# Performance work log

Measured on AMD Instinct MI355X. Metric: run time of the kernel, lower is better.

## Reference

```python
import jax, jax.numpy as jnp
import numpy as np
import math

N_CLASSES = 1000
CODE_LENGTH = 1024
IN_FEATURES = 4096
BATCH = 512
MAX_PROB = 0.95
POWER = 1.0


def _hadamard(n):
    # Sylvester construction; n must be a power of 2.
    H = np.array([[1.0]], dtype=np.float64)
    while H.shape[0] < n:
        H = np.block([[H, H], [H, -H]])
    return H


def setup_inputs() -> dict:
    key = jax.random.key(0)
    k1, k2, k3 = jax.random.split(key, 3)
    x = jax.random.normal(k1, (BATCH, IN_FEATURES), dtype=jnp.float32)
    out_feat = CODE_LENGTH - 1  # single head: code_length//1 - 1
    # nn.Linear default init: U(-1/sqrt(fan_in), 1/sqrt(fan_in))
    bound = 1.0 / math.sqrt(IN_FEATURES)
    W = jax.random.uniform(k2, (out_feat, IN_FEATURES), dtype=jnp.float32, minval=-bound, maxval=bound)
    b = jax.random.uniform(k3, (out_feat,), dtype=jnp.float32, minval=-bound, maxval=bound)
    labels = jnp.asarray(_hadamard(CODE_LENGTH)[:N_CLASSES, 1:], dtype=jnp.float32)  # (C, L-1)
    eps = jnp.float32(CODE_LENGTH * math.pow((1.0 - MAX_PROB) / (MAX_PROB * (N_CLASSES - 1)), 1.0 / POWER))
    power = jnp.float32(POWER)
    return {"x": x, "W": W, "b": b, "labels": labels, "eps": eps, "power": power}


def reference(x, W, b, labels, eps, power):
    # Linear head: (B, in) @ (in, L-1) + b
    h = jnp.tanh(x @ W.T + b)                               # (B, L-1)
    # L1 distance to each Hadamard code row: (B, 1, L-1) vs (C, L-1)
    d = jnp.sum(jnp.abs(h[:, None, :] - labels), axis=-1)   # (B, C)
    d = jnp.maximum(d, eps)
    inv = 1.0 / jnp.power(d, power)                          # (B, C)
    return inv / jnp.sum(inv, axis=-1, keepdims=True)
```

## Files before the change

### kernel.cpp

```cpp
#include <hip/hip_runtime.h>

#define BATCH 512
#define INFEAT 4096
#define LOUT 1023
#define NCLS 1000
#define NPAD 1024
#define SPLITK 8

typedef __bf16 bf16x8 __attribute__((ext_vector_type(8)));
typedef float f32x4 __attribute__((ext_vector_type(4)));

__device__ __forceinline__ unsigned short f2bf(float a) {
    unsigned u = __builtin_bit_cast(unsigned, a);
    return (unsigned short)((u + 0x7fffu + ((u >> 16) & 1u)) >> 16);
}
__device__ __forceinline__ float bf2f(unsigned short u) {
    return __builtin_bit_cast(float, ((unsigned)u) << 16);
}

__device__ __forceinline__ uint4 pack8(float4 a, float4 b) {
    union { __bf16 h[8]; uint4 u; } r;
    r.h[0] = (__bf16)a.x; r.h[1] = (__bf16)a.y;
    r.h[2] = (__bf16)a.z; r.h[3] = (__bf16)a.w;
    r.h[4] = (__bf16)b.x; r.h[5] = (__bf16)b.y;
    r.h[6] = (__bf16)b.z; r.h[7] = (__bf16)b.w;
    return r.u;
}

__global__ __launch_bounds__(256, 2) void k_gemm(
    const float* __restrict__ x, const float* __restrict__ W,
    unsigned short* __restrict__ partial) {
    __shared__ unsigned char lds[49152];
    const int bid = blockIdx.x;
    const int work = (bid & 7) * 64 + (bid >> 3);
    const int bn = work & 15, bm = (work >> 4) & 3, sp = work >> 6;
    const int tid = threadIdx.x;
    const int wave = tid >> 6, lane = tid & 63;
    const int lrow = lane & 15, lgrp = lane >> 4;
    const int wr = wave >> 1, wc = wave & 1;
    const int arow0 = bm * 128, brow0 = bn * 64, chunk0 = sp * 8;

    f32x4 acc[4][2] = {};
    float4 ar[4][2], br[2][2];

    auto LOADR = [&](int t) {
        const int c = chunk0 + t;
#pragma unroll
        for (int rr = 0; rr < 4; ++rr) {
            int g = rr * 256 + tid;
            int row = g >> 3, j = g & 7;
            const float4* p = (const float4*)(x + (size_t)(arow0 + row) * INFEAT
                                              + c * 64 + j * 8);
            ar[rr][0] = p[0]; ar[rr][1] = p[1];
        }
#pragma unroll
        for (int rr = 0; rr < 2; ++rr) {
            int g = rr * 256 + tid;
            int row = g >> 3, j = g & 7;
            int wrow = brow0 + row;
            if (wrow < LOUT) {
                const float4* p = (const float4*)(W + (size_t)wrow * INFEAT
                                                  + c * 64 + j * 8);
                br[rr][0] = p[0]; br[rr][1] = p[1];
            } else {
                br[rr][0] = make_float4(0.f, 0.f, 0.f, 0.f);
                br[rr][1] = make_float4(0.f, 0.f, 0.f, 0.f);
            }
        }
    };

    auto WRITE = [&](int bsel) {
        unsigned char* lA = lds + bsel * 24576;
        unsigned char* lB = lA + 16384;
#pragma unroll
        for (int rr = 0; rr < 4; ++rr) {
            int g = rr * 256 + tid;
            int row = g >> 3, j = g & 7;
            *(uint4*)(lA + row * 128 + ((j ^ (row & 7)) * 16)) =
                pack8(ar[rr][0], ar[rr][1]);
        }
#pragma unroll
        for (int rr = 0; rr < 2; ++rr) {
            int g = rr * 256 + tid;
            int row = g >> 3, j = g & 7;
            *(uint4*)(lB + row * 128 + ((j ^ (row & 7)) * 16)) =
                pack8(br[rr][0], br[rr][1]);
        }
    };

    auto COMPUTE = [&](int bsel) {
        const unsigned char* lA = lds + bsel * 24576;
        const unsigned char* lB = lA + 16384;
#pragma unroll
        for (int ks = 0; ks < 2; ++ks) {
            int swz = ((ks * 4 + lgrp) ^ (lrow & 7)) * 16;
            bf16x8 a[4], b[2];
#pragma unroll
            for (int m = 0; m < 4; ++m)
                a[m] = *(const bf16x8*)(lA + (wr * 64 + m * 16 + lrow) * 128 + swz);
#pragma unroll
            for (int n = 0; n < 2; ++n)
                b[n] = *(const bf16x8*)(lB + (wc * 32 + n * 16 + lrow) * 128 + swz);
#pragma unroll
            for (int m = 0; m < 4; ++m)
#pragma unroll
                for (int n = 0; n < 2; ++n)
                    acc[m][n] = __builtin_amdgcn_mfma_f32_16x16x32_bf16(
                        a[m], b[n], acc[m][n], 0, 0, 0);
        }
    };

    LOADR(0);
    WRITE(0);
    __syncthreads();
#pragma unroll 1
    for (int t = 0; t < 8; ++t) {
        if (t + 1 < 8) LOADR(t + 1);
        COMPUTE(t & 1);
        if (t + 1 < 8) WRITE((t + 1) & 1);
        __syncthreads();
    }

    unsigned short* P = partial + (size_t)sp * (BATCH * NPAD);
#pragma unroll
    for (int m = 0; m < 4; ++m)
#pragma unroll
        for (int n = 0; n < 2; ++n)
#pragma unroll
            for (int reg = 0; reg < 4; ++reg) {
                int r = arow0 + wr * 64 + m * 16 + lgrp * 4 + reg;
                int c = brow0 + wc * 32 + n * 16 + lrow;
                P[(size_t)r * NPAD + c] = f2bf(acc[m][n][reg]);
            }
}

__global__ __launch_bounds__(256) void k_fused(const unsigned short* __restrict__ partial,
                                               const float* __restrict__ bias,
                                               const float* __restrict__ epsp,
                                               const float* __restrict__ powp,
                                               float* __restrict__ out) {
    __shared__ float g[1024];
    __shared__ float wsum[4];
    const int r = blockIdx.x, t = threadIdx.x;
    const int n0 = t * 4;

    f32x4 v = {0.0f, 0.0f, 0.0f, 0.0f};
#pragma unroll
    for (int s = 0; s < SPLITK; ++s) {
        ushort4 p = *(const ushort4*)(partial + ((size_t)s * BATCH + r) * NPAD + n0);
        v[0] += bf2f(p.x); v[1] += bf2f(p.y); v[2] += bf2f(p.z); v[3] += bf2f(p.w);
    }
    float bb[4];
    if (t < 255) {
        float4 b4 = *(const float4*)(bias + n0);
        bb[0] = b4.x; bb[1] = b4.y; bb[2] = b4.z; bb[3] = b4.w;
    } else {
        bb[0] = bias[1020]; bb[1] = bias[1021]; bb[2] = bias[1022]; bb[3] = 0.0f;
    }
    if (t == 0) g[0] = 0.0f;
#pragma unroll
    for (int j = 0; j < 4; ++j) {
        int n = n0 + j;
        if (n < LOUT) g[n + 1] = tanhf(v[j] + bb[j]);
    }
    __syncthreads();

#pragma unroll 1
    for (int s = 0; s < 10; ++s) {
        int st = 1 << s;
#pragma unroll
        for (int pp = 0; pp < 2; ++pp) {
            int p = t + pp * 256;
            int idx = ((p >> s) << (s + 1)) | (p & (st - 1));
            float a = g[idx], c = g[idx + st];
            g[idx] = a + c;
            g[idx + st] = a - c;
        }
        __syncthreads();
    }

    const float eps = *epsp, pw = *powp;
    float iv[4];
    float ss = 0.0f;
#pragma unroll
    for (int j = 0; j < 4; ++j) {
        int c = n0 + j;
        float d = fmaxf(1023.0f - g[c], eps);
        float q = (pw == 1.0f) ? (1.0f / d) : powf(d, -pw);
        if (c >= NCLS) q = 0.0f;
        iv[j] = q;
        ss += q;
    }
#pragma unroll
    for (int m = 32; m; m >>= 1) ss += __shfl_xor(ss, m, 64);
    if ((t & 63) == 0) wsum[t >> 6] = ss;
    __syncthreads();
    float sc = 1.0f / (wsum[0] + wsum[1] + wsum[2] + wsum[3]);

    if (n0 < NCLS) {
        float4 o;
        o.x = iv[0] * sc; o.y = iv[1] * sc; o.z = iv[2] * sc; o.w = iv[3] * sc;
        *(float4*)(out + (size_t)r * NCLS + n0) = o;
    }
}

extern "C" void kernel_launch(void* const* d_in, const int* in_sizes, int n_in,
                              void* d_out, int out_size, void* d_ws, size_t ws_size,
                              hipStream_t stream) {
    const float* x = (const float*)d_in[0];
    const float* W = (const float*)d_in[1];
    const float* b = (const float*)d_in[2];
    const float* epsp = (const float*)d_in[4];
    const float* powp = (const float*)d_in[5];
    float* out = (float*)d_out;

    unsigned char* ws = (unsigned char*)d_ws;
    unsigned short* partial = (unsigned short*)ws;

    k_gemm<<<512, 256, 0, stream>>>(x, W, partial);
    k_fused<<<512, 256, 0, stream>>>(partial, b, epsp, powp, out);
}
```

Baseline: 26.83 us.

## Enlarge GEMM tile to 128x128 with 8 waves and three-stage register prefetch

The GEMM block grows to 512 threads covering a 128x128 output tile, which halves the grid to 256 blocks. The main loop becomes a fully unrolled schedule with two register staging sets, so global loads run two chunks ahead, fenced by explicit waitcnt, sched_barrier and s_barrier. MFMA sections are wrapped in raised s_setprio. The aim is more reuse of each A/B tile and better hiding of global load latency, at the cost of one block per CU and more registers per thread, with fewer blocks than the 256 CUs leave room to overlap.

```diff
diff --git a/kernel.cpp b/kernel.cpp
--- a/kernel.cpp
+++ b/kernel.cpp
@@ -17,7 +17,6 @@
 __device__ __forceinline__ float bf2f(unsigned short u) {
     return __builtin_bit_cast(float, ((unsigned)u) << 16);
 }
-
 __device__ __forceinline__ uint4 pack8(float4 a, float4 b) {
     union { __bf16 h[8]; uint4 u; } r;
     r.h[0] = (__bf16)a.x; r.h[1] = (__bf16)a.y;
@@ -27,70 +26,71 @@
     return r.u;
 }
 
-__global__ __launch_bounds__(256, 2) void k_gemm(
+__global__ __launch_bounds__(512, 1) void k_gemm(
     const float* __restrict__ x, const float* __restrict__ W,
     unsigned short* __restrict__ partial) {
-    __shared__ unsigned char lds[49152];
+    __shared__ unsigned char lds[65536];
     const int bid = blockIdx.x;
-    const int work = (bid & 7) * 64 + (bid >> 3);
-    const int bn = work & 15, bm = (work >> 4) & 3, sp = work >> 6;
+    const int work = (bid & 7) * 32 + (bid >> 3);
+    const int bn = work & 7, bm = (work >> 3) & 3, sp = work >> 5;
     const int tid = threadIdx.x;
     const int wave = tid >> 6, lane = tid & 63;
     const int lrow = lane & 15, lgrp = lane >> 4;
-    const int wr = wave >> 1, wc = wave & 1;
-    const int arow0 = bm * 128, brow0 = bn * 64, chunk0 = sp * 8;
+    const int wr = wave >> 2, wc = wave & 3;
+    const int arow0 = bm * 128, brow0 = bn * 128, chunk0 = sp * 8;
+
+    const int p0 = tid, p1 = 512 + tid;
+    const int row0 = p0 >> 3, jb0 = p0 & 7;
+    const int row1 = p1 >> 3, jb1 = p1 & 7;
 
     f32x4 acc[4][2] = {};
-    float4 ar[4][2], br[2][2];
-
-    auto LOADR = [&](int t) {
-        const int c = chunk0 + t;
-#pragma unroll
-        for (int rr = 0; rr < 4; ++rr) {
-            int g = rr * 256 + tid;
-            int row = g >> 3, j = g & 7;
-            const float4* p = (const float4*)(x + (size_t)(arow0 + row) * INFEAT
-                                              + c * 64 + j * 8);
-            ar[rr][0] = p[0]; ar[rr][1] = p[1];
-        }
-#pragma unroll
-        for (int rr = 0; rr < 2; ++rr) {
-            int g = rr * 256 + tid;
-            int row = g >> 3, j = g & 7;
-            int wrow = brow0 + row;
+    float4 sAa[4], sAb[4], sBa[4], sBb[4];
+
+    auto LOADR = [&](int t, float4 (&aa)[4], float4 (&bb)[4]) {
+        const size_t c0 = (size_t)(chunk0 + t) * 64;
+        {
+            const float4* q = (const float4*)(x + (size_t)(arow0 + row0) * INFEAT + c0 + jb0 * 8);
+            aa[0] = q[0]; aa[1] = q[1];
+        }
+        {
+            const float4* q = (const float4*)(x + (size_t)(arow0 + row1) * INFEAT + c0 + jb1 * 8);
+            aa[2] = q[0]; aa[3] = q[1];
+        }
+        {
+            int wrow = brow0 + row0;
             if (wrow < LOUT) {
-                const float4* p = (const float4*)(W + (size_t)wrow * INFEAT
-                                                  + c * 64 + j * 8);
-                br[rr][0] = p[0]; br[rr][1] = p[1];
+                const float4* q = (const float4*)(W + (size_t)wrow * INFEAT + c0 + jb0 * 8);
+                bb[0] = q[0]; bb[1] = q[1];
             } else {
-                br[rr][0] = make_float4(0.f, 0.f, 0.f, 0.f);
-                br[rr][1] = make_float4(0.f, 0.f, 0.f, 0.f);
+                bb[0] = make_float4(0.f, 0.f, 0.f, 0.f);
+                bb[1] = make_float4(0.f, 0.f, 0.f, 0.f);
             }
         }
+        {
+            int wrow = brow0 + row1;
+            if (wrow < LOUT) {
+                const float4* q = (const float4*)(W + (size_t)wrow * INFEAT + c0 + jb1 * 8);
+                bb[2] = q[0]; bb[3] = q[1];
+            } else {
+                bb[2] = make_float4(0.f, 0.f, 0.f, 0.f);
+                bb[3] = make_float4(0.f, 0.f, 0.f, 0.f);
+            }
+        }
     };
 
-    auto WRITE = [&](int bsel) {
-        unsigned char* lA = lds + bsel * 24576;
+    auto WRITE = [&](int bsel, float4 (&aa)[4], float4 (&bb)[4]) {
+        unsigned char* lA = lds + bsel * 32768;
         unsigned char* lB = lA + 16384;
-#pragma unroll
-        for (int rr = 0; rr < 4; ++rr) {
-            int g = rr * 256 + tid;
-            int row = g >> 3, j = g & 7;
-            *(uint4*)(lA + row * 128 + ((j ^ (row & 7)) * 16)) =
-                pack8(ar[rr][0], ar[rr][1]);
-        }
-#pragma unroll
-        for (int rr = 0; rr < 2; ++rr) {
-            int g = rr * 256 + tid;
-            int row = g >> 3, j = g & 7;
-            *(uint4*)(lB + row * 128 + ((j ^ (row & 7)) * 16)) =
-                pack8(br[rr][0], br[rr][1]);
-        }
+        *(uint4*)(lA + row0 * 128 + ((jb0 ^ (row0 & 7)) * 16)) = pack8(aa[0], aa[1]);
+        *(uint4*)(lA + row1 * 128 + ((jb1 ^ (row1 & 7)) * 16)) = pack8(aa[2], aa[3]);
+        *(uint4*)(lB + row0 * 128 + ((jb0 ^ (row0 & 7)) * 16)) = pack8(bb[0], bb[1]);
+        *(uint4*)(lB + row1 * 128 + ((jb1 ^ (row1 & 7)) * 16)) = pack8(bb[2], bb[3]);
     };
 
     auto COMPUTE = [&](int bsel) {
-        const unsigned char* lA = lds + bsel * 24576;
+        const unsigned char* lA = lds + bsel * 32768;
         const unsigned char* lB = lA + 16384;
+        __builtin_amdgcn_s_setprio(1);
 #pragma unroll
         for (int ks = 0; ks < 2; ++ks) {
             int swz = ((ks * 4 + lgrp) ^ (lrow & 7)) * 16;
@@ -108,18 +108,38 @@
                     acc[m][n] = __builtin_amdgcn_mfma_f32_16x16x32_bf16(
                         a[m], b[n], acc[m][n], 0, 0, 0);
         }
+        __builtin_amdgcn_s_setprio(0);
     };
 
-    LOADR(0);
-    WRITE(0);
-    __syncthreads();
-#pragma unroll 1
-    for (int t = 0; t < 8; ++t) {
-        if (t + 1 < 8) LOADR(t + 1);
-        COMPUTE(t & 1);
-        if (t + 1 < 8) WRITE((t + 1) & 1);
-        __syncthreads();
-    }
+    LOADR(0, sAa, sAb);
+    LOADR(1, sBa, sBb);
+    asm volatile("s_waitcnt vmcnt(8)" ::: "memory");
+    __builtin_amdgcn_sched_barrier(0);
+    WRITE(0, sAa, sAb);
+    LOADR(2, sAa, sAb);
+    asm volatile("s_waitcnt lgkmcnt(0)" ::: "memory");
+    __builtin_amdgcn_sched_barrier(0);
+    __builtin_amdgcn_s_barrier();
+
+#define STEP(T, SA, SB, VMC)                                          \
+    COMPUTE(T & 1);                                                   \
+    asm volatile("s_waitcnt vmcnt(" #VMC ")" ::: "memory");           \
+    __builtin_amdgcn_sched_barrier(0);                                \
+    WRITE((T + 1) & 1, SA, SB);                                       \
+    if ((T) <= 4) LOADR((T) + 3, SA, SB);                             \
+    asm volatile("s_waitcnt lgkmcnt(0)" ::: "memory");                \
+    __builtin_amdgcn_sched_barrier(0);                                \
+    __builtin_amdgcn_s_barrier();
+
+    STEP(0, sBa, sBb, 8)
+    STEP(1, sAa, sAb, 8)
+    STEP(2, sBa, sBb, 8)
+    STEP(3, sAa, sAb, 8)
+    STEP(4, sBa, sBb, 8)
+    STEP(5, sAa, sAb, 8)
+    STEP(6, sBa, sBb, 0)
+    COMPUTE(1);
+#undef STEP
 
     unsigned short* P = partial + (size_t)sp * (BATCH * NPAD);
 #pragma unroll
@@ -217,6 +237,6 @@
     unsigned char* ws = (unsigned char*)d_ws;
     unsigned short* partial = (unsigned short*)ws;
 
-    k_gemm<<<512, 256, 0, stream>>>(x, W, partial);
+    k_gemm<<<256, 512, 0, stream>>>(x, W, partial);
     k_fused<<<512, 256, 0, stream>>>(partial, b, epsp, powp, out);
 }
```

New measurement: 25.92 us. -3.4%, faster.

## Stage full W slice in LDS once and stream x fragments directly into registers

Applied to the files above, without the earlier changes.

The GEMM kernel now uses 256 blocks of 512 threads, each with a 128x128 output tile over a 512-wide K slice. The whole bf16 W slice (128 KB) is loaded into LDS up front with one barrier. The x operand is loaded straight from global memory into MFMA fragment registers, using a three-deep register prefetch ring. This removes the per-step LDS double-buffering and its barriers, at the cost of occupancy limited to one block per CU, a large LDS footprint, and uncoalesced per-lane x loads that each block re-reads from global memory.

```diff
diff --git a/kernel.cpp b/kernel.cpp
--- a/kernel.cpp
+++ b/kernel.cpp
@@ -6,6 +6,8 @@
 #define NCLS 1000
 #define NPAD 1024
 #define SPLITK 8
+#define KSLICE 512
+#define NCHUNK 16
 
 typedef __bf16 bf16x8 __attribute__((ext_vector_type(8)));
 typedef float f32x4 __attribute__((ext_vector_type(4)));
@@ -17,109 +19,88 @@
 __device__ __forceinline__ float bf2f(unsigned short u) {
     return __builtin_bit_cast(float, ((unsigned)u) << 16);
 }
-
-__device__ __forceinline__ uint4 pack8(float4 a, float4 b) {
-    union { __bf16 h[8]; uint4 u; } r;
+__device__ __forceinline__ bf16x8 pack8(float4 a, float4 b) {
+    union { __bf16 h[8]; bf16x8 v; } r;
     r.h[0] = (__bf16)a.x; r.h[1] = (__bf16)a.y;
     r.h[2] = (__bf16)a.z; r.h[3] = (__bf16)a.w;
     r.h[4] = (__bf16)b.x; r.h[5] = (__bf16)b.y;
     r.h[6] = (__bf16)b.z; r.h[7] = (__bf16)b.w;
-    return r.u;
-}
-
-__global__ __launch_bounds__(256, 2) void k_gemm(
+    return r.v;
+}
+
+__global__ __launch_bounds__(512, 1) void k_gemm(
     const float* __restrict__ x, const float* __restrict__ W,
     unsigned short* __restrict__ partial) {
-    __shared__ unsigned char lds[49152];
+    __shared__ unsigned char lB[128 * 1024];
     const int bid = blockIdx.x;
-    const int work = (bid & 7) * 64 + (bid >> 3);
-    const int bn = work & 15, bm = (work >> 4) & 3, sp = work >> 6;
+    const int work = (bid & 7) * 32 + (bid >> 3);
+    const int bn = work & 7, bm = (work >> 3) & 3, sp = work >> 5;
     const int tid = threadIdx.x;
     const int wave = tid >> 6, lane = tid & 63;
     const int lrow = lane & 15, lgrp = lane >> 4;
-    const int wr = wave >> 1, wc = wave & 1;
-    const int arow0 = bm * 128, brow0 = bn * 64, chunk0 = sp * 8;
+    const int wr = wave >> 2, wc = wave & 3;
+    const int arow0 = bm * 128, brow0 = bn * 128;
+    const size_t c0 = (size_t)sp * KSLICE;
+
+    {
+        const int r = tid >> 2, s = tid & 3;
+        const int wrow = brow0 + r;
+        const float* src = W + (size_t)wrow * INFEAT + c0 + s * 128;
+        unsigned char* dst = lB + r * 1024;
+#pragma unroll
+        for (int i = 0; i < 16; ++i) {
+            float4 v0, v1;
+            if (wrow < LOUT) {
+                v0 = *(const float4*)(src + i * 8);
+                v1 = *(const float4*)(src + i * 8 + 4);
+            } else {
+                v0 = make_float4(0.f, 0.f, 0.f, 0.f);
+                v1 = v0;
+            }
+            *(bf16x8*)(dst + (((s * 16 + i) ^ (r & 7)) * 16)) = pack8(v0, v1);
+        }
+    }
+    __syncthreads();
 
     f32x4 acc[4][2] = {};
-    float4 ar[4][2], br[2][2];
-
-    auto LOADR = [&](int t) {
-        const int c = chunk0 + t;
-#pragma unroll
-        for (int rr = 0; rr < 4; ++rr) {
-            int g = rr * 256 + tid;
-            int row = g >> 3, j = g & 7;
-            const float4* p = (const float4*)(x + (size_t)(arow0 + row) * INFEAT
-                                              + c * 64 + j * 8);
-            ar[rr][0] = p[0]; ar[rr][1] = p[1];
-        }
-#pragma unroll
-        for (int rr = 0; rr < 2; ++rr) {
-            int g = rr * 256 + tid;
-            int row = g >> 3, j = g & 7;
-            int wrow = brow0 + row;
-            if (wrow < LOUT) {
-                const float4* p = (const float4*)(W + (size_t)wrow * INFEAT
-                                                  + c * 64 + j * 8);
-                br[rr][0] = p[0]; br[rr][1] = p[1];
-            } else {
-                br[rr][0] = make_float4(0.f, 0.f, 0.f, 0.f);
-                br[rr][1] = make_float4(0.f, 0.f, 0.f, 0.f);
-            }
+    float4 A0[4][2], A1[4][2], A2[4][2];
+
+    auto LOADA = [&](int kk, float4 (&S)[4][2]) {
+#pragma unroll
+        for (int m = 0; m < 4; ++m) {
+            const float4* q = (const float4*)(x +
+                (size_t)(arow0 + wr * 64 + m * 16 + lrow) * INFEAT +
+                c0 + kk * 32 + lgrp * 8);
+            S[m][0] = q[0]; S[m][1] = q[1];
         }
     };
 
-    auto WRITE = [&](int bsel) {
-        unsigned char* lA = lds + bsel * 24576;
-        unsigned char* lB = lA + 16384;
-#pragma unroll
-        for (int rr = 0; rr < 4; ++rr) {
-            int g = rr * 256 + tid;
-            int row = g >> 3, j = g & 7;
-            *(uint4*)(lA + row * 128 + ((j ^ (row & 7)) * 16)) =
-                pack8(ar[rr][0], ar[rr][1]);
-        }
-#pragma unroll
-        for (int rr = 0; rr < 2; ++rr) {
-            int g = rr * 256 + tid;
-            int row = g >> 3, j = g & 7;
-            *(uint4*)(lB + row * 128 + ((j ^ (row & 7)) * 16)) =
-                pack8(br[rr][0], br[rr][1]);
-        }
-    };
-
-    auto COMPUTE = [&](int bsel) {
-        const unsigned char* lA = lds + bsel * 24576;
-        const unsigned char* lB = lA + 16384;
-#pragma unroll
-        for (int ks = 0; ks < 2; ++ks) {
-            int swz = ((ks * 4 + lgrp) ^ (lrow & 7)) * 16;
-            bf16x8 a[4], b[2];
-#pragma unroll
-            for (int m = 0; m < 4; ++m)
-                a[m] = *(const bf16x8*)(lA + (wr * 64 + m * 16 + lrow) * 128 + swz);
-#pragma unroll
-            for (int n = 0; n < 2; ++n)
-                b[n] = *(const bf16x8*)(lB + (wc * 32 + n * 16 + lrow) * 128 + swz);
-#pragma unroll
-            for (int m = 0; m < 4; ++m)
-#pragma unroll
-                for (int n = 0; n < 2; ++n)
-                    acc[m][n] = __builtin_amdgcn_mfma_f32_16x16x32_bf16(
-                        a[m], b[n], acc[m][n], 0, 0, 0);
-        }
-    };
-
-    LOADR(0);
-    WRITE(0);
-    __syncthreads();
-#pragma unroll 1
-    for (int t = 0; t < 8; ++t) {
-        if (t + 1 < 8) LOADR(t + 1);
-        COMPUTE(t & 1);
-        if (t + 1 < 8) WRITE((t + 1) & 1);
-        __syncthreads();
-    }
+#define STEP(KK, SCUR)                                                        \
+    {                                                                         \
+        bf16x8 a[4], b[2];                                                    \
+        _Pragma("unroll")                                                     \
+        for (int m = 0; m < 4; ++m) a[m] = pack8(SCUR[m][0], SCUR[m][1]);     \
+        _Pragma("unroll")                                                     \
+        for (int n = 0; n < 2; ++n)                                           \
+            b[n] = *(const bf16x8*)(lB + (wc * 32 + n * 16 + lrow) * 1024 +   \
+                                    ((((KK) * 4 + lgrp) ^ (lrow & 7)) * 16)); \
+        if ((KK) + 3 < NCHUNK) LOADA((KK) + 3, SCUR);                         \
+        _Pragma("unroll")                                                     \
+        for (int m = 0; m < 4; ++m)                                           \
+            _Pragma("unroll")                                                 \
+            for (int n = 0; n < 2; ++n)                                       \
+                acc[m][n] = __builtin_amdgcn_mfma_f32_16x16x32_bf16(          \
+                    a[m], b[n], acc[m][n], 0, 0, 0);                          \
+    }
+
+    LOADA(0, A0); LOADA(1, A1); LOADA(2, A2);
+    STEP(0, A0)  STEP(1, A1)  STEP(2, A2)
+    STEP(3, A0)  STEP(4, A1)  STEP(5, A2)
+    STEP(6, A0)  STEP(7, A1)  STEP(8, A2)
+    STEP(9, A0)  STEP(10, A1) STEP(11, A2)
+    STEP(12, A0) STEP(13, A1) STEP(14, A2)
+    STEP(15, A0)
+#undef STEP
 
     unsigned short* P = partial + (size_t)sp * (BATCH * NPAD);
 #pragma unroll
@@ -217,6 +198,6 @@
     unsigned char* ws = (unsigned char*)d_ws;
     unsigned short* partial = (unsigned short*)ws;
 
-    k_gemm<<<512, 256, 0, stream>>>(x, W, partial);
+    k_gemm<<<256, 512, 0, stream>>>(x, W, partial);
     k_fused<<<512, 256, 0, stream>>>(partial, b, epsp, powp, out);
 }
```

Result: slower. 51.72 us (+92.8%).
